# Kernel optimization log

Hardware: AMD Instinct MI355X
Metric: run time of the kernel (lower is better)

Reference implementation:

```python
import jax, jax.numpy as jnp
import numpy as np

B, L, H, T_MAX, D_ID, D_SZ, D_POS = 64, 1024, 256, 128, 128, 64, 128
V_ID, V_SZ = 65536, 256


def setup_inputs() -> dict:
    key = jax.random.key(0)
    ks = jax.random.split(key, 16)
    s = 0.02
    inp = {
        'obj_id': jax.random.randint(ks[0], (B,), 0, V_ID, dtype=jnp.int32),
        'obj_size': jax.random.randint(ks[1], (B,), 0, V_SZ, dtype=jnp.int32),
        'cache_lines': jax.random.randint(ks[2], (B, L), 0, V_ID, dtype=jnp.int32),
        'lengths': jax.random.randint(ks[3], (B,), 0, L, dtype=jnp.int32),
        'c0': jax.random.normal(ks[4], (B, H), jnp.float32),
        'h0': jax.random.normal(ks[5], (B, H), jnp.float32),
        'history': jax.random.normal(ks[6], (B, T_MAX - 1, H), jnp.float32),
        # learned parameters
        'obj_id_table': jax.random.normal(ks[7], (V_ID, D_ID), jnp.float32) * s,
        'obj_size_table': jax.random.normal(ks[8], (V_SZ, D_SZ), jnp.float32) * s,
        'pos_table': jax.random.normal(ks[9], (T_MAX, D_POS), jnp.float32) * s,
        'W_ih': jax.random.normal(ks[10], (4 * H, D_ID + D_SZ), jnp.float32) * s,
        'W_hh': jax.random.normal(ks[11], (4 * H, H), jnp.float32) * s,
        'b_ih': jnp.zeros((4 * H,), jnp.float32),
        'b_hh': jnp.zeros((4 * H,), jnp.float32),
        'attn_W': jax.random.normal(ks[12], (D_ID, H), jnp.float32) * s,
        'scorer_W': jax.random.normal(ks[13], (1, H + D_POS), jnp.float32) * s,
        'scorer_b': jnp.zeros((1,), jnp.float32),
        'reuse_W': jax.random.normal(ks[14], (1, H + D_POS), jnp.float32) * s,
        'reuse_b': jnp.zeros((1,), jnp.float32),
    }
    return inp


def reference(obj_id, obj_size, cache_lines, lengths, c0, h0, history,
              obj_id_table, obj_size_table, pos_table,
              W_ih, W_hh, b_ih, b_hh, attn_W,
              scorer_W, scorer_b, reuse_W, reuse_b):
    # --- embed current access and run one LSTMCell step ---
    x = jnp.concatenate([obj_id_table[obj_id], obj_size_table[obj_size]], axis=-1)  # (B, D_ID+D_SZ)
    gates = x @ W_ih.T + b_ih + h0 @ W_hh.T + b_hh  # (B, 4H)
    i, f, g, o = jnp.split(gates, 4, axis=-1)
    c = jax.nn.sigmoid(f) * c0 + jax.nn.sigmoid(i) * jnp.tanh(g)
    h = jax.nn.sigmoid(o) * jnp.tanh(c)

    # --- growing hidden-state history (deque bounded at max_attention_history) ---
    hist = jnp.concatenate([history, h[:, None, :]], axis=1)  # (B, T, H)
    T = hist.shape[1]
    pos = jnp.broadcast_to(pos_table[:T][None], (hist.shape[0], T, pos_table.shape[1]))
    values = jnp.concatenate([hist, pos], axis=-1)  # (B, T, H+P)

    # --- cache line embeddings (cache_lines_embedder == obj_id_embedder) ---
    q = obj_id_table[cache_lines]  # (B, L, D_ID)

    # --- General (bilinear) multi-query attention over history ---
    scores = jnp.einsum('bld,dh,bth->blt', q, attn_W, hist)  # (B, L, T)
    weights = jax.nn.softmax(scores, axis=-1)
    contexts = jnp.einsum('blt,btv->blv', weights, values)  # (B, L, H+P)

    # --- heads ---
    line_scores = jax.nn.softmax((contexts @ scorer_W.T + scorer_b)[..., 0], axis=-1)  # (B, L)
    pred_reuse = (contexts @ reuse_W.T + reuse_b)[..., 0]  # (B, L)

    # --- mask_renormalize over valid (unpadded) cache lines ---
    valid = jnp.maximum(lengths, 1)[:, None]  # min_len=1 in pad()
    mask = (jnp.arange(line_scores.shape[1])[None, :] < valid).astype(line_scores.dtype)
    masked = line_scores * mask
    denom = masked.sum(axis=-1, keepdims=True)
    probs = masked / jnp.where(denom > 0, denom, 1.0)
    return probs, pred_reuse
```

## Files before the change

kernel.cpp:

```cpp
#include <hip/hip_runtime.h>
#include <math.h>

#define BB 64
#define LL 1024
#define HH 256
#define TT 128
#define D_ID 128
#define D_SZ 64
#define D_POS 128
#define DX 192

typedef short s16x8 __attribute__((ext_vector_type(8)));
typedef float f32x16 __attribute__((ext_vector_type(16)));
typedef unsigned short u16x8 __attribute__((ext_vector_type(8)));

__device__ __forceinline__ unsigned short f2bf(float f) {
    unsigned u = __float_as_uint(f);
    unsigned r = u + 0x7fffu + ((u >> 16) & 1u);
    return (unsigned short)(r >> 16);
}

__device__ __forceinline__ s16x8 pack8(float4 a, float4 b) {
    u16x8 p;
    p[0] = f2bf(a.x); p[1] = f2bf(a.y); p[2] = f2bf(a.z); p[3] = f2bf(a.w);
    p[4] = f2bf(b.x); p[5] = f2bf(b.y); p[6] = f2bf(b.z); p[7] = f2bf(b.w);
    return (s16x8)p;
}

__global__ void embed_kernel(const int* __restrict__ obj_id,
                             const int* __restrict__ obj_size,
                             const float* __restrict__ h0,
                             const float* __restrict__ obj_id_table,
                             const float* __restrict__ obj_size_table,
                             float* __restrict__ xh_t,
                             unsigned short* __restrict__ qT) {
    int blk = blockIdx.x;
    int tid = threadIdx.x;

    if (blk < 112) {
        int b = tid & 63;
        int k = blk * 4 + (tid >> 6);
        float v;
        if (k < D_ID)      v = obj_id_table[(size_t)obj_id[b] * D_ID + k];
        else if (k < DX)   v = obj_size_table[(size_t)obj_size[b] * D_SZ + (k - D_ID)];
        else               v = h0[b * HH + (k - DX)];
        xh_t[k * 64 + b] = v;
        return;
    }

    size_t g = ((size_t)(blk - 112) * 256 + tid) * 8;
    float4 a = *(const float4*)(obj_id_table + g);
    float4 b = *(const float4*)(obj_id_table + g + 4);
    *(s16x8*)(qT + g) = pack8(a, b);
}

__global__ void gates_kernel(const float* __restrict__ xh_t,
                             const float* __restrict__ W_ih,
                             const float* __restrict__ W_hh,
                             const float* __restrict__ b_ih,
                             const float* __restrict__ b_hh,
                             const float* __restrict__ c0,
                             float* __restrict__ h_new) {
    int j = blockIdx.x;
    int tid = threadIdx.x;
    int b = tid & 63;
    int q = __builtin_amdgcn_readfirstlane(tid >> 6);
    int r = q * HH + j;
    __shared__ float gS[256];

    float acc = b_ih[r] + b_hh[r];
    const float* wi = W_ih + (size_t)r * DX;
    const float* wh = W_hh + (size_t)r * HH;
#pragma unroll 16
    for (int k = 0; k < DX; ++k)
        acc += wi[k] * xh_t[k * 64 + b];
#pragma unroll 16
    for (int k = 0; k < HH; ++k)
        acc += wh[k] * xh_t[(DX + k) * 64 + b];
    gS[q * 64 + b] = acc;
    __syncthreads();

    if (tid < 64) {
        float ig = 1.f / (1.f + expf(-gS[tid]));
        float fg = 1.f / (1.f + expf(-gS[64 + tid]));
        float gg = tanhf(gS[128 + tid]);
        float og = 1.f / (1.f + expf(-gS[192 + tid]));
        float c = fg * c0[tid * HH + j] + ig * gg;
        h_new[tid * HH + j] = og * tanhf(c);
    }
}

__global__ void proj_kernel(const float* __restrict__ history,
                            const float* __restrict__ h_new,
                            const float* __restrict__ attn_W,
                            const float* __restrict__ pos_table,
                            const float* __restrict__ scorer_W,
                            const float* __restrict__ reuse_W,
                            unsigned short* __restrict__ hp,
                            float* __restrict__ sv,
                            float* __restrict__ rv) {
    int blk = blockIdx.x;
    int tid = threadIdx.x;

    if (blk >= BB * 16) {
        int idx = blk - BB * 16;
        int b = idx >> 2;
        int which = (idx >> 1) & 1;
        int t = (idx & 1) * 64 + tid;
        const float* w = which ? reuse_W : scorer_W;
        const float* hrow = (t < TT - 1)
            ? history + ((size_t)b * (TT - 1) + t) * HH
            : h_new + (size_t)b * HH;
        float acc = 0.f;
#pragma unroll 8
        for (int k = 0; k < HH / 4; ++k) {
            float4 hv = *(const float4*)(hrow + 4 * k);
            float4 wv = *(const float4*)(w + 4 * k);
            acc += hv.x * wv.x + hv.y * wv.y + hv.z * wv.z + hv.w * wv.w;
        }
        const float* prow = pos_table + (size_t)t * D_POS;
#pragma unroll 8
        for (int k = 0; k < D_POS / 4; ++k) {
            float4 pv = *(const float4*)(prow + 4 * k);
            float4 wv = *(const float4*)(w + HH + 4 * k);
            acc += pv.x * wv.x + pv.y * wv.y + pv.z * wv.z + pv.w * wv.w;
        }
        (which ? rv : sv)[b * TT + t] = acc;
        return;
    }

    int b  = blk >> 4;
    int t0 = ((blk >> 2) & 3) * 32;
    int d0 = (blk & 3) * 32;
    int lane = tid;
    int ln = lane & 31, half = lane >> 5;

    int t = t0 + ln;
    const float* arow = (t < TT - 1)
        ? history + ((size_t)b * (TT - 1) + t) * HH
        : h_new + (size_t)b * HH;
    const float* brow = attn_W + (size_t)(d0 + ln) * HH;

    f32x16 acc;
#pragma unroll
    for (int r = 0; r < 16; ++r) acc[r] = 0.f;

#pragma unroll
    for (int ks = 0; ks < 16; ++ks) {
        int off = ks * 16 + half * 8;
        float4 a0 = *(const float4*)(arow + off);
        float4 a1 = *(const float4*)(arow + off + 4);
        float4 b0 = *(const float4*)(brow + off);
        float4 b1 = *(const float4*)(brow + off + 4);
        acc = __builtin_amdgcn_mfma_f32_32x32x16_bf16(
            pack8(a0, a1), pack8(b0, b1), acc, 0, 0, 0);
    }

#pragma unroll
    for (int r = 0; r < 16; ++r) {
        int tt = t0 + (r & 3) + 8 * (r >> 2) + 4 * half;
        hp[((size_t)b * TT + tt) * D_ID + d0 + ln] = f2bf(acc[r]);
    }
}

__global__ void __launch_bounds__(64, 2)
attn_kernel(const int* __restrict__ cache_lines,
            const unsigned short* __restrict__ qT,
            const unsigned short* __restrict__ hp,
            const float* __restrict__ sv,
            const float* __restrict__ rv,
            const float* __restrict__ scorer_b,
            const float* __restrict__ reuse_b,
            float* __restrict__ logits,
            float* __restrict__ out_reuse) {
    int b  = blockIdx.x >> 5;
    int l0 = (blockIdx.x & 31) * 32;
    int lane = threadIdx.x;
    int ln = lane & 31, half = lane >> 5;

    int cl = cache_lines[b * LL + l0 + ln];
    const unsigned short* qrow = qT + (size_t)cl * D_ID + half * 8;
    s16x8 qf[8];
#pragma unroll
    for (int ks = 0; ks < 8; ++ks)
        qf[ks] = *(const s16x8*)(qrow + ks * 16);

    float sv_r[4], rv_r[4];
#pragma unroll
    for (int tt = 0; tt < 4; ++tt) {
        sv_r[tt] = sv[b * TT + tt * 32 + ln];
        rv_r[tt] = rv[b * TT + tt * 32 + ln];
    }
    float sb = scorer_b[0], rb = reuse_b[0];

    const unsigned short* hpb = hp + (size_t)b * TT * D_ID + half * 8;
    f32x16 acc[4];
#pragma unroll
    for (int tt = 0; tt < 4; ++tt)
#pragma unroll
        for (int r = 0; r < 16; ++r) acc[tt][r] = 0.f;

#pragma unroll
    for (int k = 0; k < 8; ++k) {
#pragma unroll
        for (int tt = 0; tt < 4; ++tt) {
            s16x8 bf = *(const s16x8*)(hpb + (size_t)(tt * 32 + ln) * D_ID + k * 16);
            acc[tt] = __builtin_amdgcn_mfma_f32_32x32x16_bf16(qf[k], bf, acc[tt], 0, 0, 0);
        }
    }

#pragma unroll
    for (int r = 0; r < 16; ++r) {
        float v0 = acc[0][r], v1 = acc[1][r], v2 = acc[2][r], v3 = acc[3][r];
        float m = fmaxf(fmaxf(v0, v1), fmaxf(v2, v3));
#pragma unroll
        for (int off = 1; off < 32; off <<= 1) m = fmaxf(m, __shfl_xor(m, off));
        float e0 = __expf(v0 - m), e1 = __expf(v1 - m),
              e2 = __expf(v2 - m), e3 = __expf(v3 - m);
        float s  = e0 + e1 + e2 + e3;
        float lg = e0 * sv_r[0] + e1 * sv_r[1] + e2 * sv_r[2] + e3 * sv_r[3];
        float rg = e0 * rv_r[0] + e1 * rv_r[1] + e2 * rv_r[2] + e3 * rv_r[3];
#pragma unroll
        for (int off = 1; off < 32; off <<= 1) {
            s  += __shfl_xor(s, off);
            lg += __shfl_xor(lg, off);
            rg += __shfl_xor(rg, off);
        }
        if (ln == 0) {
            int row = (r & 3) + 8 * (r >> 2) + 4 * half;
            int l = l0 + row;
            logits[b * LL + l] = lg / s + sb;
            out_reuse[b * LL + l] = rg / s + rb;
        }
    }
}

__global__ void finalsm_kernel(const float* __restrict__ logits,
                               const int* __restrict__ lengths,
                               float* __restrict__ out_probs) {
    int b = blockIdx.x;
    int tid = threadIdx.x;
    int valid = max(lengths[b], 1);
    float v[4];
    float m = -1e30f;
#pragma unroll
    for (int i = 0; i < 4; ++i) {
        int l = tid + 256 * i;
        v[i] = (l < valid) ? logits[b * LL + l] : -1e30f;
        m = fmaxf(m, v[i]);
    }
#pragma unroll
    for (int off = 1; off < 64; off <<= 1) m = fmaxf(m, __shfl_xor(m, off));
    __shared__ float redm[4];
    __shared__ float reds[4];
    int wave = tid >> 6;
    if ((tid & 63) == 0) redm[wave] = m;
    __syncthreads();
    m = fmaxf(fmaxf(redm[0], redm[1]), fmaxf(redm[2], redm[3]));
    float e[4];
    float s = 0.f;
#pragma unroll
    for (int i = 0; i < 4; ++i) {
        int l = tid + 256 * i;
        e[i] = (l < valid) ? expf(v[i] - m) : 0.f;
        s += e[i];
    }
#pragma unroll
    for (int off = 1; off < 64; off <<= 1) s += __shfl_xor(s, off);
    if ((tid & 63) == 0) reds[wave] = s;
    __syncthreads();
    s = reds[0] + reds[1] + reds[2] + reds[3];
    float inv = 1.f / s;
#pragma unroll
    for (int i = 0; i < 4; ++i)
        out_probs[b * LL + tid + 256 * i] = e[i] * inv;
}

extern "C" void kernel_launch(void* const* d_in, const int* in_sizes, int n_in,
                              void* d_out, int out_size, void* d_ws, size_t ws_size,
                              hipStream_t stream) {
    const int*   obj_id         = (const int*)d_in[0];
    const int*   obj_size       = (const int*)d_in[1];
    const int*   cache_lines    = (const int*)d_in[2];
    const int*   lengths        = (const int*)d_in[3];
    const float* c0             = (const float*)d_in[4];
    const float* h0             = (const float*)d_in[5];
    const float* history        = (const float*)d_in[6];
    const float* obj_id_table   = (const float*)d_in[7];
    const float* obj_size_table = (const float*)d_in[8];
    const float* pos_table      = (const float*)d_in[9];
    const float* W_ih           = (const float*)d_in[10];
    const float* W_hh           = (const float*)d_in[11];
    const float* b_ih           = (const float*)d_in[12];
    const float* b_hh           = (const float*)d_in[13];
    const float* attn_W         = (const float*)d_in[14];
    const float* scorer_W       = (const float*)d_in[15];
    const float* scorer_b       = (const float*)d_in[16];
    const float* reuse_W        = (const float*)d_in[17];
    const float* reuse_b        = (const float*)d_in[18];

    float* out = (float*)d_out;
    float* out_probs = out;
    float* out_reuse = out + BB * LL;

    char* ws = (char*)d_ws;
    float*          h_new  = (float*)(ws);
    unsigned short* hp     = (unsigned short*)(ws + 65536);
    float*          sv     = (float*)(ws + 2162688);
    float*          rv     = (float*)(ws + 2195456);
    float*          xh_t   = (float*)(ws + 2228224);
    float*          logits = (float*)(ws + 2228224);
    unsigned short* qT     = (unsigned short*)(ws + 4194304);

    hipLaunchKernelGGL(embed_kernel, dim3(112 + 4096), dim3(256), 0, stream,
                       obj_id, obj_size, h0, obj_id_table, obj_size_table,
                       xh_t, qT);
    hipLaunchKernelGGL(gates_kernel, dim3(HH), dim3(256), 0, stream,
                       xh_t, W_ih, W_hh, b_ih, b_hh, c0, h_new);
    hipLaunchKernelGGL(proj_kernel, dim3(BB * 16 + BB * 4), dim3(64), 0, stream,
                       history, h_new, attn_W, pos_table, scorer_W, reuse_W,
                       hp, sv, rv);
    hipLaunchKernelGGL(attn_kernel, dim3(BB * 32), dim3(64), 0, stream,
                       cache_lines, qT, hp, sv, rv,
                       scorer_b, reuse_b, logits, out_reuse);
    hipLaunchKernelGGL(finalsm_kernel, dim3(BB), dim3(256), 0, stream,
                       logits, lengths, out_probs);
}
```

Before: 167.0 us.

## Pre-pack projected history into MFMA fragment layout and swap attention operands

History, attn_W and h_new are now converted to bf16 in earlier kernels. The projection kernel writes its output in a fragment-ordered layout, so the attention kernel can load each B operand as one contiguous 16-byte vector per lane. The attention MFMA operands are swapped so each lane owns a single query row across T. This turns the per-row 32-lane shuffle reductions into one cross-half shuffle and lets sv/rv be read as float4. The cost is extra workspace, an additional bf16 conversion pass over history, and a proj kernel with fewer, larger blocks.

New measurement: 171.8 us. 2.9% more time.

```diff
diff --git a/kernel.cpp b/kernel.cpp
--- a/kernel.cpp
+++ b/kernel.cpp
@@ -13,6 +13,7 @@
 typedef short s16x8 __attribute__((ext_vector_type(8)));
 typedef float f32x16 __attribute__((ext_vector_type(16)));
 typedef unsigned short u16x8 __attribute__((ext_vector_type(8)));
+typedef unsigned short u16x4 __attribute__((ext_vector_type(4)));
 
 __device__ __forceinline__ unsigned short f2bf(float f) {
     unsigned u = __float_as_uint(f);
@@ -32,8 +33,12 @@
                              const float* __restrict__ h0,
                              const float* __restrict__ obj_id_table,
                              const float* __restrict__ obj_size_table,
+                             const float* __restrict__ history,
+                             const float* __restrict__ attn_W,
                              float* __restrict__ xh_t,
-                             unsigned short* __restrict__ qT) {
+                             unsigned short* __restrict__ qT,
+                             unsigned short* __restrict__ histB,
+                             unsigned short* __restrict__ attnWB) {
     int blk = blockIdx.x;
     int tid = threadIdx.x;
 
@@ -47,11 +52,26 @@
         xh_t[k * 64 + b] = v;
         return;
     }
-
-    size_t g = ((size_t)(blk - 112) * 256 + tid) * 8;
-    float4 a = *(const float4*)(obj_id_table + g);
-    float4 b = *(const float4*)(obj_id_table + g + 4);
-    *(s16x8*)(qT + g) = pack8(a, b);
+    if (blk < 4208) {
+        size_t g = ((size_t)(blk - 112) * 256 + tid) * 8;
+        float4 a = *(const float4*)(obj_id_table + g);
+        float4 b = *(const float4*)(obj_id_table + g + 4);
+        *(s16x8*)(qT + g) = pack8(a, b);
+        return;
+    }
+    if (blk < 5224) {
+        size_t g = ((size_t)(blk - 4208) * 256 + tid) * 8;
+        float4 a = *(const float4*)(history + g);
+        float4 b = *(const float4*)(history + g + 4);
+        *(s16x8*)(histB + g) = pack8(a, b);
+        return;
+    }
+    {
+        size_t g = ((size_t)(blk - 5224) * 256 + tid) * 8;
+        float4 a = *(const float4*)(attn_W + g);
+        float4 b = *(const float4*)(attn_W + g + 4);
+        *(s16x8*)(attnWB + g) = pack8(a, b);
+    }
 }
 
 __global__ void gates_kernel(const float* __restrict__ xh_t,
@@ -60,7 +80,8 @@
                              const float* __restrict__ b_ih,
                              const float* __restrict__ b_hh,
                              const float* __restrict__ c0,
-                             float* __restrict__ h_new) {
+                             float* __restrict__ h_new,
+                             unsigned short* __restrict__ hnewB) {
     int j = blockIdx.x;
     int tid = threadIdx.x;
     int b = tid & 63;
@@ -86,27 +107,30 @@
         float gg = tanhf(gS[128 + tid]);
         float og = 1.f / (1.f + expf(-gS[192 + tid]));
         float c = fg * c0[tid * HH + j] + ig * gg;
-        h_new[tid * HH + j] = og * tanhf(c);
-    }
-}
-
-__global__ void proj_kernel(const float* __restrict__ history,
+        float h = og * tanhf(c);
+        h_new[tid * HH + j] = h;
+        hnewB[tid * HH + j] = f2bf(h);
+    }
+}
+
+__global__ void proj_kernel(const unsigned short* __restrict__ histB,
+                            const unsigned short* __restrict__ hnewB,
+                            const float* __restrict__ history,
                             const float* __restrict__ h_new,
-                            const float* __restrict__ attn_W,
+                            const unsigned short* __restrict__ attnWB,
                             const float* __restrict__ pos_table,
                             const float* __restrict__ scorer_W,
                             const float* __restrict__ reuse_W,
-                            unsigned short* __restrict__ hp,
+                            unsigned short* __restrict__ hpF,
                             float* __restrict__ sv,
                             float* __restrict__ rv) {
     int blk = blockIdx.x;
     int tid = threadIdx.x;
 
-    if (blk >= BB * 16) {
-        int idx = blk - BB * 16;
-        int b = idx >> 2;
-        int which = (idx >> 1) & 1;
-        int t = (idx & 1) * 64 + tid;
+    if (blk >= 256) {
+        int b = blk - 256;
+        int which = tid >> 7;
+        int t = tid & 127;
         const float* w = which ? reuse_W : scorer_W;
         const float* hrow = (t < TT - 1)
             ? history + ((size_t)b * (TT - 1) + t) * HH
@@ -129,17 +153,17 @@
         return;
     }
 
-    int b  = blk >> 4;
-    int t0 = ((blk >> 2) & 3) * 32;
-    int d0 = (blk & 3) * 32;
-    int lane = tid;
+    int b  = blk >> 2;
+    int tt = blk & 3;
+    int w  = tid >> 6;
+    int lane = tid & 63;
     int ln = lane & 31, half = lane >> 5;
 
-    int t = t0 + ln;
-    const float* arow = (t < TT - 1)
-        ? history + ((size_t)b * (TT - 1) + t) * HH
-        : h_new + (size_t)b * HH;
-    const float* brow = attn_W + (size_t)(d0 + ln) * HH;
+    int t = tt * 32 + ln;
+    const unsigned short* arow = attnWB + (size_t)(32 * w + ln) * HH;
+    const unsigned short* brow = (t < TT - 1)
+        ? histB + ((size_t)b * (TT - 1) + t) * HH
+        : hnewB + (size_t)b * HH;
 
     f32x16 acc;
 #pragma unroll
@@ -148,25 +172,29 @@
 #pragma unroll
     for (int ks = 0; ks < 16; ++ks) {
         int off = ks * 16 + half * 8;
-        float4 a0 = *(const float4*)(arow + off);
-        float4 a1 = *(const float4*)(arow + off + 4);
-        float4 b0 = *(const float4*)(brow + off);
-        float4 b1 = *(const float4*)(brow + off + 4);
-        acc = __builtin_amdgcn_mfma_f32_32x32x16_bf16(
-            pack8(a0, a1), pack8(b0, b1), acc, 0, 0, 0);
-    }
-
-#pragma unroll
-    for (int r = 0; r < 16; ++r) {
-        int tt = t0 + (r & 3) + 8 * (r >> 2) + 4 * half;
-        hp[((size_t)b * TT + tt) * D_ID + d0 + ln] = f2bf(acc[r]);
-    }
-}
-
-__global__ void __launch_bounds__(64, 2)
+        s16x8 af = *(const s16x8*)(arow + off);
+        s16x8 bf = *(const s16x8*)(brow + off);
+        acc = __builtin_amdgcn_mfma_f32_32x32x16_bf16(af, bf, acc, 0, 0, 0);
+    }
+
+    unsigned short* hb = hpF + (size_t)b * 16384;
+#pragma unroll
+    for (int qd = 0; qd < 4; ++qd) {
+        u16x4 v;
+        v[0] = f2bf(acc[4 * qd + 0]);
+        v[1] = f2bf(acc[4 * qd + 1]);
+        v[2] = f2bf(acc[4 * qd + 2]);
+        v[3] = f2bf(acc[4 * qd + 3]);
+        int sa = ((2 * w + (qd >> 1)) * 4 + tt) * 512 +
+                 (qd & 1) * 256 + ln * 8 + 4 * half;
+        *(u16x4*)(hb + sa) = v;
+    }
+}
+
+__global__ void __launch_bounds__(64)
 attn_kernel(const int* __restrict__ cache_lines,
             const unsigned short* __restrict__ qT,
-            const unsigned short* __restrict__ hp,
+            const unsigned short* __restrict__ hpF,
             const float* __restrict__ sv,
             const float* __restrict__ rv,
             const float* __restrict__ scorer_b,
@@ -185,53 +213,54 @@
     for (int ks = 0; ks < 8; ++ks)
         qf[ks] = *(const s16x8*)(qrow + ks * 16);
 
-    float sv_r[4], rv_r[4];
+    float sb = scorer_b[0], rb = reuse_b[0];
+
+    const s16x8* hpb = (const s16x8*)(hpF) + (size_t)b * 2048;
+    f32x16 acc[4];
+#pragma unroll
+    for (int tt = 0; tt < 4; ++tt)
+#pragma unroll
+        for (int r = 0; r < 16; ++r) acc[tt][r] = 0.f;
+
+#pragma unroll
+    for (int k = 0; k < 8; ++k) {
+#pragma unroll
+        for (int tt = 0; tt < 4; ++tt) {
+            s16x8 bf = hpb[(k * 4 + tt) * 64 + lane];
+            acc[tt] = __builtin_amdgcn_mfma_f32_32x32x16_bf16(bf, qf[k], acc[tt], 0, 0, 0);
+        }
+    }
+
+    float m = -1e30f;
+#pragma unroll
+    for (int tt = 0; tt < 4; ++tt)
+#pragma unroll
+        for (int r = 0; r < 16; ++r) m = fmaxf(m, acc[tt][r]);
+    m = fmaxf(m, __shfl_xor(m, 32));
+
+    float s = 0.f, lg = 0.f, rg = 0.f;
 #pragma unroll
     for (int tt = 0; tt < 4; ++tt) {
-        sv_r[tt] = sv[b * TT + tt * 32 + ln];
-        rv_r[tt] = rv[b * TT + tt * 32 + ln];
-    }
-    float sb = scorer_b[0], rb = reuse_b[0];
-
-    const unsigned short* hpb = hp + (size_t)b * TT * D_ID + half * 8;
-    f32x16 acc[4];
-#pragma unroll
-    for (int tt = 0; tt < 4; ++tt)
-#pragma unroll
-        for (int r = 0; r < 16; ++r) acc[tt][r] = 0.f;
-
-#pragma unroll
-    for (int k = 0; k < 8; ++k) {
-#pragma unroll
-        for (int tt = 0; tt < 4; ++tt) {
-            s16x8 bf = *(const s16x8*)(hpb + (size_t)(tt * 32 + ln) * D_ID + k * 16);
-            acc[tt] = __builtin_amdgcn_mfma_f32_32x32x16_bf16(qf[k], bf, acc[tt], 0, 0, 0);
+#pragma unroll
+        for (int q = 0; q < 4; ++q) {
+            const float4 s4 = *(const float4*)(sv + b * TT + tt * 32 + 8 * q + 4 * half);
+            const float4 r4 = *(const float4*)(rv + b * TT + tt * 32 + 8 * q + 4 * half);
+            float e0 = __expf(acc[tt][4 * q + 0] - m);
+            float e1 = __expf(acc[tt][4 * q + 1] - m);
+            float e2 = __expf(acc[tt][4 * q + 2] - m);
+            float e3 = __expf(acc[tt][4 * q + 3] - m);
+            s  += e0 + e1 + e2 + e3;
+            lg += e0 * s4.x + e1 * s4.y + e2 * s4.z + e3 * s4.w;
+            rg += e0 * r4.x + e1 * r4.y + e2 * r4.z + e3 * r4.w;
         }
     }
-
-#pragma unroll
-    for (int r = 0; r < 16; ++r) {
-        float v0 = acc[0][r], v1 = acc[1][r], v2 = acc[2][r], v3 = acc[3][r];
-        float m = fmaxf(fmaxf(v0, v1), fmaxf(v2, v3));
-#pragma unroll
-        for (int off = 1; off < 32; off <<= 1) m = fmaxf(m, __shfl_xor(m, off));
-        float e0 = __expf(v0 - m), e1 = __expf(v1 - m),
-              e2 = __expf(v2 - m), e3 = __expf(v3 - m);
-        float s  = e0 + e1 + e2 + e3;
-        float lg = e0 * sv_r[0] + e1 * sv_r[1] + e2 * sv_r[2] + e3 * sv_r[3];
-        float rg = e0 * rv_r[0] + e1 * rv_r[1] + e2 * rv_r[2] + e3 * rv_r[3];
-#pragma unroll
-        for (int off = 1; off < 32; off <<= 1) {
-            s  += __shfl_xor(s, off);
-            lg += __shfl_xor(lg, off);
-            rg += __shfl_xor(rg, off);
-        }
-        if (ln == 0) {
-            int row = (r & 3) + 8 * (r >> 2) + 4 * half;
-            int l = l0 + row;
-            logits[b * LL + l] = lg / s + sb;
-            out_reuse[b * LL + l] = rg / s + rb;
-        }
+    s  += __shfl_xor(s, 32);
+    lg += __shfl_xor(lg, 32);
+    rg += __shfl_xor(rg, 32);
+
+    if (half == 0) {
+        logits[b * LL + l0 + ln] = lg / s + sb;
+        out_reuse[b * LL + l0 + ln] = rg / s + rb;
     }
 }
 
@@ -305,23 +334,26 @@
 
     char* ws = (char*)d_ws;
     float*          h_new  = (float*)(ws);
-    unsigned short* hp     = (unsigned short*)(ws + 65536);
+    unsigned short* hpF    = (unsigned short*)(ws + 65536);
     float*          sv     = (float*)(ws + 2162688);
     float*          rv     = (float*)(ws + 2195456);
     float*          xh_t   = (float*)(ws + 2228224);
     float*          logits = (float*)(ws + 2228224);
     unsigned short* qT     = (unsigned short*)(ws + 4194304);
-
-    hipLaunchKernelGGL(embed_kernel, dim3(112 + 4096), dim3(256), 0, stream,
+    unsigned short* histB  = (unsigned short*)(ws + 20971520);
+    unsigned short* attnWB = (unsigned short*)(ws + 25165824);
+    unsigned short* hnewB  = (unsigned short*)(ws + 25231360);
+
+    hipLaunchKernelGGL(embed_kernel, dim3(5240), dim3(256), 0, stream,
                        obj_id, obj_size, h0, obj_id_table, obj_size_table,
-                       xh_t, qT);
+                       history, attn_W, xh_t, qT, histB, attnWB);
     hipLaunchKernelGGL(gates_kernel, dim3(HH), dim3(256), 0, stream,
-                       xh_t, W_ih, W_hh, b_ih, b_hh, c0, h_new);
-    hipLaunchKernelGGL(proj_kernel, dim3(BB * 16 + BB * 4), dim3(64), 0, stream,
-                       history, h_new, attn_W, pos_table, scorer_W, reuse_W,
-                       hp, sv, rv);
+                       xh_t, W_ih, W_hh, b_ih, b_hh, c0, h_new, hnewB);
+    hipLaunchKernelGGL(proj_kernel, dim3(320), dim3(256), 0, stream,
+                       histB, hnewB, history, h_new, attnWB, pos_table,
+                       scorer_W, reuse_W, hpF, sv, rv);
     hipLaunchKernelGGL(attn_kernel, dim3(BB * 32), dim3(64), 0, stream,
-                       cache_lines, qT, hp, sv, rv,
+                       cache_lines, qT, hpF, sv, rv,
                        scorer_b, reuse_b, logits, out_reuse);
     hipLaunchKernelGGL(finalsm_kernel, dim3(BB), dim3(256), 0, stream,
                        logits, lengths, out_probs);
```
